# Kernel optimization log

Measured on AMD Instinct MI355X. Metric: run time of the kernel, lower is better.

## Reference

```python
import jax, jax.numpy as jnp
import numpy as np

SEGMENT_LENGTHS = [2048, 4096, 8192]
DILATION_RATES = [1, 2, 4]
BATCH, SEQ_LEN, HEADS, HEAD_DIM = 1, 8192, 16, 64
SCALE = HEAD_DIM ** (-0.5)


def _hilbert_index_to_xy(index, n):
    # Exact replica of the torch module's integer Hilbert d->(x,y) mapping.
    x = y = 0
    s = 1
    while s < n:
        rx = 1 & (index // 2)
        ry = 1 & (index ^ rx)
        if ry == 0:
            if rx == 1:
                x, y = s - 1 - y, s - 1 - x
            x, y = y, x
        x += s * rx
        y += s * ry
        index //= 4
        s *= 2
    return x, y


def _hilbert_perm(n):
    # Replicates _generate_hilbert_indices, including the fill-in tail and
    d = 1
    while d * d < n:
        d *= 2
    idx = []
    for i in range(min(n, d * d)):
        x, y = _hilbert_index_to_xy(i, d)
        p = x * d + y
        if p < n:
            idx.append(p)
    if len(idx) < n:
        idx.extend(range(len(idx), n))
    perm = np.array(idx[:n], dtype=np.int64)
    inv = np.zeros(n, dtype=np.int64)
    inv[perm] = np.arange(n, dtype=np.int64)
    return perm, inv


_PERM_CACHE = {}


def _get_perm(n):
    if n not in _PERM_CACHE:
        _PERM_CACHE[n] = _hilbert_perm(n)
    return _PERM_CACHE[n]


def setup_inputs() -> dict:
    key = jax.random.key(0)
    kq, kk, kv = jax.random.split(key, 3)
    shape = (BATCH, SEQ_LEN, HEADS, HEAD_DIM)
    return {
        "q": jax.random.normal(kq, shape, dtype=jnp.float32),
        "k": jax.random.normal(kk, shape, dtype=jnp.float32),
        "v": jax.random.normal(kv, shape, dtype=jnp.float32),
    }


def reference(q, k, v) -> jnp.ndarray:
    B, L, H, D = q.shape
    n_groups = len(SEGMENT_LENGTHS)
    heads_per_group = max(1, H // n_groups)
    out = jnp.zeros_like(q)
    for g, (seg_len, dil) in enumerate(zip(SEGMENT_LENGTHS, DILATION_RATES)):
        S = min(seg_len, L)
        h0 = g * heads_per_group
        if h0 >= H:
            continue
        h1 = min(h0 + heads_per_group, H)
        assert L % S == 0, "seq_len must tile into segments"
        N = L // S  # number of segments
        Hg = h1 - h0
        # [B, N, S, Hg, D]
        qg = q[:, :, h0:h1].reshape(B, N, S, Hg, D)
        kg = k[:, :, h0:h1].reshape(B, N, S, Hg, D)
        vg = v[:, :, h0:h1].reshape(B, N, S, Hg, D)
        if S > 64:
            perm, inv = _get_perm(S)
        else:
            perm = np.arange(S, dtype=np.int64)
            inv = perm
        # dilation applied AFTER Hilbert ordering -> compose the gathers
        kv_idx = perm[np.arange(0, S, dil)]
        qp = qg[:, :, perm]           # [B,N,S,Hg,D]
        kd = kg[:, :, kv_idx]         # [B,N,S/dil,Hg,D]
        vd = vg[:, :, kv_idx]
        scores = jnp.einsum('bnqhd,bnkhd->bnhqk', qp, kd) * SCALE
        attn = jnp.nan_to_num(jax.nn.softmax(scores, axis=-1))
        og = jnp.einsum('bnhqk,bnkhd->bnqhd', attn, vd)  # [B,N,S,Hg,D]
        og = og[:, :, inv]            # inverse Hilbert scatter
        out = out.at[:, :, h0:h1].set(og.reshape(B, L, Hg, D))
    return out
```

## Files before the change

kernel.cpp:

```cpp
#include <hip/hip_runtime.h>
#include <hip/hip_bf16.h>

typedef __attribute__((ext_vector_type(8))) short bf16x8;
typedef __attribute__((ext_vector_type(16))) float f32x16;
typedef __attribute__((ext_vector_type(2))) unsigned u32x2;

#define LDKP 72

__device__ __forceinline__ unsigned pk2(float a, float b) {
    union { __hip_bfloat162 h2; unsigned u; } c;
    c.h2 = __float22bfloat162_rn(make_float2(a, b));
    return c.u;
}

__device__ __forceinline__ void gld16(const void* g, void* l) {
    __builtin_amdgcn_global_load_lds(
        (const __attribute__((address_space(1))) unsigned*)g,
        (__attribute__((address_space(3))) unsigned*)l, 16, 0, 0);
}

__device__ inline int hilbert_p(int index, int d) {
    int x = 0, y = 0;
    for (int s = 1; s < d; s <<= 1) {
        int rx = (index >> 1) & 1;
        int ry = (index ^ rx) & 1;
        if (ry == 0) {
            if (rx == 1) {
                int nx = s - 1 - y;
                int ny = s - 1 - x;
                x = nx; y = ny;
            }
            int t = x; x = y; y = t;
        }
        x += s * rx;
        y += s * ry;
        index >>= 2;
    }
    return x * d + y;
}

__global__ __launch_bounds__(256) void gather_kv(
    const float* __restrict__ K, const float* __restrict__ V,
    short* __restrict__ Kp, short* __restrict__ Vp)
{
    __shared__ short vt[64 * LDKP];

    const int b = blockIdx.x;
    int g, rb;
    if (b < 640)      { g = 0; rb = b; }
    else if (b < 960) { g = 1; rb = b - 640; }
    else              { g = 2; rb = b - 960; }
    const int nseg   = 4 >> g;
    const int hl     = rb / (nseg * 32);
    const int r2     = rb - hl * (nseg * 32);
    const int seg    = r2 >> 5;
    const int kt     = r2 & 31;
    const int h      = g * 5 + hl;
    const int S      = 2048 << g;
    const int segrow = seg * S;
    const int dgrid  = (g == 2) ? 128 : 64;
    const size_t tile_s = (size_t)b * 4096;

    for (int it = threadIdx.x; it < 512; it += 256) {
        const int j  = it >> 3;
        const int c8 = it & 7;
        const int ii = kt * 64 + j;
        const int p  = (g == 0) ? ii : hilbert_p(ii << g, dgrid);
        const size_t src = ((size_t)((segrow + p) * 16 + h)) * 64 + c8 * 8;
        const float4* kp = (const float4*)(K + src);
        const float4* vp = (const float4*)(V + src);
        float4 k0 = kp[0], k1 = kp[1];
        float4 v0 = vp[0], v1 = vp[1];
        union { unsigned u[4]; bf16x8 v; } ck, cv;
        ck.u[0] = pk2(k0.x, k0.y); ck.u[1] = pk2(k0.z, k0.w);
        ck.u[2] = pk2(k1.x, k1.y); ck.u[3] = pk2(k1.z, k1.w);
        cv.u[0] = pk2(v0.x, v0.y); cv.u[1] = pk2(v0.z, v0.w);
        cv.u[2] = pk2(v1.x, v1.y); cv.u[3] = pk2(v1.z, v1.w);
        const int kchunk = ((j >> 5) * 4 + (c8 >> 1)) * 64 + (c8 & 1) * 32 + (j & 31);
        *(bf16x8*)&Kp[tile_s + kchunk * 8] = ck.v;
        *(bf16x8*)&vt[j * LDKP + ((c8 ^ (j >> 3)) * 8)] = cv.v;
    }
    __syncthreads();
    for (int it = threadIdx.x; it < 512; it += 256) {
        const int dd = it >> 3;
        const int k8 = it & 7;
        union { short s[8]; bf16x8 v; } o;
#pragma unroll
        for (int u = 0; u < 8; ++u)
            o.s[u] = vt[(k8 * 8 + u) * LDKP + (((dd >> 3) ^ k8) * 8) + (dd & 7)];
        const int vchunk = ((k8 >> 1) * 2 + (dd >> 5)) * 64 + (k8 & 1) * 32 + (dd & 31);
        *(bf16x8*)&Vp[tile_s + vchunk * 8] = o.v;
    }
}

__global__ __launch_bounds__(256, 4) void attn_kernel(
    const float* __restrict__ Q, float* __restrict__ O,
    const short* __restrict__ Kp, const short* __restrict__ Vp)
{
    __shared__ __align__(16) short ldsK[2][4096];
    __shared__ __align__(16) short ldsV[2][4096];

    const int bx = blockIdx.x;
    const int g  = bx / 320;
    const int r  = bx - g * 320;
    const int hl = r >> 6;
    const int qb = r & 63;
    const int h  = g * 5 + hl;
    const int qglob = qb * 128;
    const int seg   = qb >> (4 + g);
    const int tile0 = ((g == 0) ? 0 : (g == 1) ? 640 : 960) + (hl * (4 >> g) + seg) * 32;

    const int tid  = threadIdx.x;
    const int wave = tid >> 6;
    const int lane = tid & 63;
    const int l31  = lane & 31;
    const int hi   = lane >> 5;

    if (g == 0 && hl == 0) {
        const float4 z = make_float4(0.f, 0.f, 0.f, 0.f);
        for (int i = tid; i < 2048; i += 256) {
            int row = qglob + (i >> 4);
            ((float4*)O)[(size_t)(row * 16 + 15) * 16 + (i & 15)] = z;
        }
    }

    const float cs = 0.125f * 1.44269504088896f;
    bf16x8 qf[4];
    {
        const int qrow = qglob + wave * 32 + l31;
        const float* qp = Q + ((size_t)(qrow * 16 + h)) * 64;
#pragma unroll
        for (int ks = 0; ks < 4; ++ks) {
            const float4* p4 = (const float4*)(qp + ks * 16 + hi * 8);
            float4 a = p4[0], b = p4[1];
            union { unsigned u[4]; bf16x8 v; } f;
            f.u[0] = pk2(a.x * cs, a.y * cs); f.u[1] = pk2(a.z * cs, a.w * cs);
            f.u[2] = pk2(b.x * cs, b.y * cs); f.u[3] = pk2(b.z * cs, b.w * cs);
            qf[ks] = f.v;
        }
    }

    f32x16 oacc[2];
#pragma unroll
    for (int rr = 0; rr < 16; ++rr) { oacc[0][rr] = 0.f; oacc[1][rr] = 0.f; }
    float lp = 0.f;

    const int lbase = lane * 8;

    {
        const size_t tb = (size_t)tile0 << 13;
        const char* kgp = (const char*)Kp + tb + (wave << 11) + (lane << 4);
        const char* vgp = (const char*)Vp + tb + (wave << 11) + (lane << 4);
        char* klp = (char*)&ldsK[0][0] + (wave << 11);
        char* vlp = (char*)&ldsV[0][0] + (wave << 11);
        gld16(kgp,        klp);
        gld16(kgp + 1024, klp + 1024);
        gld16(vgp,        vlp);
        gld16(vgp + 1024, vlp + 1024);
    }

    for (int kt = 0; kt < 32; ++kt) {
        const int cur = kt & 1;
        if (kt < 31) {
            const size_t tb = (size_t)(tile0 + kt + 1) << 13;
            const char* kgp = (const char*)Kp + tb + (wave << 11) + (lane << 4);
            const char* vgp = (const char*)Vp + tb + (wave << 11) + (lane << 4);
            char* klp = (char*)&ldsK[cur ^ 1][0] + (wave << 11);
            char* vlp = (char*)&ldsV[cur ^ 1][0] + (wave << 11);
            gld16(kgp,        klp);
            gld16(kgp + 1024, klp + 1024);
            gld16(vgp,        vlp);
            gld16(vgp + 1024, vlp + 1024);
            asm volatile("s_waitcnt vmcnt(4)" ::: "memory");
        } else {
            asm volatile("s_waitcnt vmcnt(0)" ::: "memory");
        }
        asm volatile("s_barrier" ::: "memory");

        const short* lK = &ldsK[cur][lbase];
        const short* lV = &ldsV[cur][lbase];

        float lacc = 0.f;
        unsigned dw[16];
        __builtin_amdgcn_s_setprio(1);
#pragma unroll
        for (int kb = 0; kb < 2; ++kb) {
            bf16x8 kf0 = *(const bf16x8*)&lK[(kb * 4 + 0) * 512];
            bf16x8 kf1 = *(const bf16x8*)&lK[(kb * 4 + 1) * 512];
            bf16x8 kf2 = *(const bf16x8*)&lK[(kb * 4 + 2) * 512];
            bf16x8 kf3 = *(const bf16x8*)&lK[(kb * 4 + 3) * 512];
            f32x16 sa;
#pragma unroll
            for (int rr = 0; rr < 16; ++rr) sa[rr] = 0.f;
            sa = __builtin_amdgcn_mfma_f32_32x32x16_bf16(kf0, qf[0], sa, 0, 0, 0);
            sa = __builtin_amdgcn_mfma_f32_32x32x16_bf16(kf1, qf[1], sa, 0, 0, 0);
            sa = __builtin_amdgcn_mfma_f32_32x32x16_bf16(kf2, qf[2], sa, 0, 0, 0);
            sa = __builtin_amdgcn_mfma_f32_32x32x16_bf16(kf3, qf[3], sa, 0, 0, 0);
            float pe[16];
#pragma unroll
            for (int rr = 0; rr < 16; ++rr) pe[rr] = __builtin_amdgcn_exp2f(sa[rr]);
            lacc += (((pe[0] + pe[1]) + (pe[2] + pe[3])) + ((pe[4] + pe[5]) + (pe[6] + pe[7])))
                  + (((pe[8] + pe[9]) + (pe[10] + pe[11])) + ((pe[12] + pe[13]) + (pe[14] + pe[15])));
#pragma unroll
            for (int kslo = 0; kslo < 2; ++kslo)
#pragma unroll
                for (int j = 0; j < 2; ++j)
#pragma unroll
                    for (int hT = 0; hT < 2; ++hT) {
                        const int r0 = 2 * j + 8 * kslo + 4 * hT;
                        dw[(kb * 2 + kslo) * 4 + j * 2 + hT] = pk2(pe[r0], pe[r0 + 1]);
                    }
        }
        __builtin_amdgcn_s_setprio(0);
        lp += lacc;

        bf16x8 pa[4];
#pragma unroll
        for (int ks = 0; ks < 4; ++ks) {
            u32x2 r0 = __builtin_amdgcn_permlane32_swap(dw[ks * 4 + 0], dw[ks * 4 + 1], false, false);
            u32x2 r1 = __builtin_amdgcn_permlane32_swap(dw[ks * 4 + 2], dw[ks * 4 + 3], false, false);
            union { unsigned u[4]; bf16x8 v; } p;
            p.u[0] = r0[0]; p.u[1] = r1[0]; p.u[2] = r0[1]; p.u[3] = r1[1];
            pa[ks] = p.v;
        }

        __builtin_amdgcn_sched_barrier(0);

        bf16x8 vf[4][2];
#pragma unroll
        for (int ks = 0; ks < 4; ++ks)
#pragma unroll
            for (int db = 0; db < 2; ++db)
                vf[ks][db] = *(const bf16x8*)&lV[(ks * 2 + db) * 512];

        __builtin_amdgcn_s_setprio(1);
#pragma unroll
        for (int ks = 0; ks < 4; ++ks) {
            oacc[0] = __builtin_amdgcn_mfma_f32_32x32x16_bf16(pa[ks], vf[ks][0], oacc[0], 0, 0, 0);
            oacc[1] = __builtin_amdgcn_mfma_f32_32x32x16_bf16(pa[ks], vf[ks][1], oacc[1], 0, 0, 0);
        }
        __builtin_amdgcn_s_setprio(0);

        asm volatile("s_barrier" ::: "memory");
    }

    float ltot = lp + __shfl_xor(lp, 32, 64);
    float linv = 1.0f / ltot;

#pragma unroll
    for (int rr = 0; rr < 16; ++rr) {
        const int m = (rr & 3) + ((rr >> 2) << 3) + (hi << 2);
        float inv = __shfl(linv, m, 64);
        const int qrow = qglob + wave * 32 + m;
        float* op = O + ((size_t)(qrow * 16 + h)) * 64 + l31;
        op[0]  = oacc[0][rr] * inv;
        op[32] = oacc[1][rr] * inv;
    }
}

extern "C" void kernel_launch(void* const* d_in, const int* in_sizes, int n_in,
                              void* d_out, int out_size, void* d_ws, size_t ws_size,
                              hipStream_t stream) {
    const float* q = (const float*)d_in[0];
    const float* k = (const float*)d_in[1];
    const float* v = (const float*)d_in[2];
    float* out = (float*)d_out;
    short* Kp = (short*)d_ws;
    short* Vp = Kp + (size_t)1120 * 4096;

    gather_kv<<<1120, 256, 0, stream>>>(k, v, Kp, Vp);
    attn_kernel<<<960, 256, 0, stream>>>(q, out, Kp, Vp);
}
```

Measured before the change: 204.1 us.

## Transpose V tiles in registers and split gather warps between K and V

The gather kernel no longer stages V through a shared-memory tile with a barrier. One wave of 64 threads now loads 8x8 fp32 blocks of V into registers and transposes them in place. The other three waves convert and write K. This removes the LDS round trip and __syncthreads, but leaves the work unbalanced: one wave carries all of V (8 rows of 8 floats per thread) while 192 threads share K. That could lengthen each block's critical path and raise register pressure.

Measured after the change: 207.8 us. Within noise of the previous version (+1.8%).

```diff
diff --git a/kernel.cpp b/kernel.cpp
--- a/kernel.cpp
+++ b/kernel.cpp
@@ -4,8 +4,6 @@
 typedef __attribute__((ext_vector_type(8))) short bf16x8;
 typedef __attribute__((ext_vector_type(16))) float f32x16;
 typedef __attribute__((ext_vector_type(2))) unsigned u32x2;
-
-#define LDKP 72
 
 __device__ __forceinline__ unsigned pk2(float a, float b) {
     union { __hip_bfloat162 h2; unsigned u; } c;
@@ -39,12 +37,10 @@
     return x * d + y;
 }
 
-__global__ __launch_bounds__(256) void gather_kv(
+__global__ __launch_bounds__(256, 4) void gather_kv(
     const float* __restrict__ K, const float* __restrict__ V,
     short* __restrict__ Kp, short* __restrict__ Vp)
 {
-    __shared__ short vt[64 * LDKP];
-
     const int b = blockIdx.x;
     int g, rb;
     if (b < 640)      { g = 0; rb = b; }
@@ -61,35 +57,49 @@
     const int dgrid  = (g == 2) ? 128 : 64;
     const size_t tile_s = (size_t)b * 4096;
 
-    for (int it = threadIdx.x; it < 512; it += 256) {
-        const int j  = it >> 3;
-        const int c8 = it & 7;
-        const int ii = kt * 64 + j;
-        const int p  = (g == 0) ? ii : hilbert_p(ii << g, dgrid);
-        const size_t src = ((size_t)((segrow + p) * 16 + h)) * 64 + c8 * 8;
-        const float4* kp = (const float4*)(K + src);
-        const float4* vp = (const float4*)(V + src);
-        float4 k0 = kp[0], k1 = kp[1];
-        float4 v0 = vp[0], v1 = vp[1];
-        union { unsigned u[4]; bf16x8 v; } ck, cv;
-        ck.u[0] = pk2(k0.x, k0.y); ck.u[1] = pk2(k0.z, k0.w);
-        ck.u[2] = pk2(k1.x, k1.y); ck.u[3] = pk2(k1.z, k1.w);
-        cv.u[0] = pk2(v0.x, v0.y); cv.u[1] = pk2(v0.z, v0.w);
-        cv.u[2] = pk2(v1.x, v1.y); cv.u[3] = pk2(v1.z, v1.w);
-        const int kchunk = ((j >> 5) * 4 + (c8 >> 1)) * 64 + (c8 & 1) * 32 + (j & 31);
-        *(bf16x8*)&Kp[tile_s + kchunk * 8] = ck.v;
-        *(bf16x8*)&vt[j * LDKP + ((c8 ^ (j >> 3)) * 8)] = cv.v;
-    }
-    __syncthreads();
-    for (int it = threadIdx.x; it < 512; it += 256) {
-        const int dd = it >> 3;
-        const int k8 = it & 7;
-        union { short s[8]; bf16x8 v; } o;
-#pragma unroll
-        for (int u = 0; u < 8; ++u)
-            o.s[u] = vt[(k8 * 8 + u) * LDKP + (((dd >> 3) ^ k8) * 8) + (dd & 7)];
-        const int vchunk = ((k8 >> 1) * 2 + (dd >> 5)) * 64 + (k8 & 1) * 32 + (dd & 31);
-        *(bf16x8*)&Vp[tile_s + vchunk * 8] = o.v;
+    const int tid = threadIdx.x;
+
+    if (tid < 64) {
+        const int k8 = tid >> 3;
+        const int d8 = tid & 7;
+        float rowf[8][8];
+#pragma unroll
+        for (int u = 0; u < 8; ++u) {
+            const int j  = k8 * 8 + u;
+            const int ii = kt * 64 + j;
+            const int p  = (g == 0) ? ii : hilbert_p(ii << g, dgrid);
+            const float* vp = V + ((size_t)((segrow + p) * 16 + h)) * 64 + d8 * 8;
+            float4 a = ((const float4*)vp)[0];
+            float4 bq = ((const float4*)vp)[1];
+            rowf[u][0] = a.x;  rowf[u][1] = a.y;  rowf[u][2] = a.z;  rowf[u][3] = a.w;
+            rowf[u][4] = bq.x; rowf[u][5] = bq.y; rowf[u][6] = bq.z; rowf[u][7] = bq.w;
+        }
+#pragma unroll
+        for (int w = 0; w < 8; ++w) {
+            const int dd = d8 * 8 + w;
+            union { unsigned u4[4]; bf16x8 v; } o;
+            o.u4[0] = pk2(rowf[0][w], rowf[1][w]);
+            o.u4[1] = pk2(rowf[2][w], rowf[3][w]);
+            o.u4[2] = pk2(rowf[4][w], rowf[5][w]);
+            o.u4[3] = pk2(rowf[6][w], rowf[7][w]);
+            const int vchunk = ((k8 >> 1) * 2 + (dd >> 5)) * 64 + (k8 & 1) * 32 + (dd & 31);
+            *(bf16x8*)&Vp[tile_s + vchunk * 8] = o.v;
+        }
+    } else {
+        for (int it = tid - 64; it < 512; it += 192) {
+            const int j  = it >> 3;
+            const int c8 = it & 7;
+            const int ii = kt * 64 + j;
+            const int p  = (g == 0) ? ii : hilbert_p(ii << g, dgrid);
+            const float* kp = K + ((size_t)((segrow + p) * 16 + h)) * 64 + c8 * 8;
+            float4 k0 = ((const float4*)kp)[0];
+            float4 k1 = ((const float4*)kp)[1];
+            union { unsigned u4[4]; bf16x8 v; } ck;
+            ck.u4[0] = pk2(k0.x, k0.y); ck.u4[1] = pk2(k0.z, k0.w);
+            ck.u4[2] = pk2(k1.x, k1.y); ck.u4[3] = pk2(k1.z, k1.w);
+            const int kchunk = ((j >> 5) * 4 + (c8 >> 1)) * 64 + (c8 & 1) * 32 + (j & 31);
+            *(bf16x8*)&Kp[tile_s + kchunk * 8] = ck.v;
+        }
     }
 }
 
```
